# Kernel tuning notes

Hardware: AMD Instinct MI355X
Metric: run time of the kernel (lower is better)

The kernel has to match this reference:

```python
import jax, jax.numpy as jnp
import numpy as np


def _gru_layer(x, h0, W_ih, W_hh, b_ih, b_hh):
    """PyTorch-convention GRU layer.
    x: [B, T, F], h0: [B, H], W_ih: [3H, F], W_hh: [3H, H], biases: [3H].
    Gate order (torch): r, z, n.  Returns (out [B,T,H], hT [B,H]).
    """
    # Precompute input projections for all timesteps in one big GEMM.
    gx = jnp.einsum('btf,gf->btg', x, W_ih) + b_ih  # [B, T, 3H]
    gx = jnp.swapaxes(gx, 0, 1)  # [T, B, 3H] for scan

    def step(h, gx_t):
        gh = h @ W_hh.T + b_hh                      # [B, 3H]
        xr, xz, xn = jnp.split(gx_t, 3, axis=-1)
        hr, hz, hn = jnp.split(gh, 3, axis=-1)
        r = jax.nn.sigmoid(xr + hr)
        z = jax.nn.sigmoid(xz + hz)
        n = jnp.tanh(xn + r * hn)
        h_new = (1.0 - z) * n + z * h
        return h_new, h_new

    hT, outs = jax.lax.scan(step, h0, gx)
    return jnp.swapaxes(outs, 0, 1), hT  # [B, T, H], [B, H]


def setup_inputs() -> dict:
    key = jax.random.key(0)
    ks = jax.random.split(key, 12)
    B, T, F, H, O = 256, 2000, 80, 64, 29
    s = 1.0 / np.sqrt(H)  # torch GRU/Linear init scale ~ U(-1/sqrt(H), 1/sqrt(H))
    u = lambda k, shp: jax.random.uniform(k, shp, jnp.float32, -s, s)
    return {
        'x': jax.random.normal(ks[0], (B, T, F), jnp.float32),
        'h': jnp.zeros((2, B, H), jnp.float32),
        'W_ih0': u(ks[1], (3 * H, F)),
        'W_hh0': u(ks[2], (3 * H, H)),
        'b_ih0': u(ks[3], (3 * H,)),
        'b_hh0': u(ks[4], (3 * H,)),
        'W_ih1': u(ks[5], (3 * H, H)),
        'W_hh1': u(ks[6], (3 * H, H)),
        'b_ih1': u(ks[7], (3 * H,)),
        'b_hh1': u(ks[8], (3 * H,)),
        'W_fc': u(ks[9], (O, H)),
        'b_fc': u(ks[10], (O,)),
    }


def reference(x, h, W_ih0, W_hh0, b_ih0, b_hh0, W_ih1, W_hh1, b_ih1, b_hh1, W_fc, b_fc):
    # Layer 0
    out0, h0T = _gru_layer(x, h[0], W_ih0, W_hh0, b_ih0, b_hh0)
    # Layer 1 (inter-layer dropout disabled: inference / eval mode)
    out1, h1T = _gru_layer(out0, h[1], W_ih1, W_hh1, b_ih1, b_hh1)
    hidden_state = jnp.stack([h0T, h1T], axis=0)  # [num_layers, B, H]
    # fc(relu(output[:, -1]))
    logits = jax.nn.relu(out1[:, -1]) @ W_fc.T + b_fc  # [B, O]
    return logits, hidden_state
```

## Files before the change

kernel.cpp:

```cpp
#include <hip/hip_runtime.h>

#define T_STEPS 2000
#define BATCH   256
#define F_IN    80
#define HDIM    64

template<int N> struct IC { static constexpr int v = N; };

typedef _Float16 h2 __attribute__((ext_vector_type(2)));
typedef _Float16 h4 __attribute__((ext_vector_type(4)));
typedef _Float16 h8 __attribute__((ext_vector_type(8)));

union U8 { h8 v; h2 p[4]; };
union U4 { h4 v; h2 p[2]; };

__device__ __forceinline__ float sigm_f(float v) {
    float e = __expf(-v);
    return __builtin_amdgcn_rcpf(1.f + e);
}
__device__ __forceinline__ float tanh_f(float v) {
    v = fminf(fmaxf(v, -15.f), 15.f);
    float e = __expf(-2.f * v);
    return (1.f - e) * __builtin_amdgcn_rcpf(1.f + e);
}
__device__ __forceinline__ float qred(float v) {
    v += __int_as_float(__builtin_amdgcn_mov_dpp(__float_as_int(v), 0xB1, 0xF, 0xF, true));
    v += __int_as_float(__builtin_amdgcn_mov_dpp(__float_as_int(v), 0x4E, 0xF, 0xF, true));
    return v;
}
__device__ __forceinline__ void barrier_lds() {
    __builtin_amdgcn_s_waitcnt(0xC07F);
    __builtin_amdgcn_s_barrier();
}
__device__ __forceinline__ float fdot2(h2 a, h2 b, float c) {
    return __builtin_amdgcn_fdot2(a, b, c, false);
}
__device__ __forceinline__ h2 mk2(float a, float b) {
    h2 r; r.x = (_Float16)a; r.y = (_Float16)b; return r;
}

__global__ __launch_bounds__(512, 2)
void gru_fused(const float* __restrict__ x,
               const float* __restrict__ hin,
               const float* __restrict__ Wih0,
               const float* __restrict__ Whh0,
               const float* __restrict__ bih0, const float* __restrict__ bhh0,
               const float* __restrict__ Wih1,
               const float* __restrict__ Whh1,
               const float* __restrict__ bih1, const float* __restrict__ bhh1,
               float* __restrict__ out_hidden)
{
    const int b    = blockIdx.x;
    const int tid  = threadIdx.x;
    const int lane = tid & 63;
    const int w    = tid >> 6;
    const bool isL1 = (w >= 4);
    const int ks   = lane & 3;
    const int gg   = lane >> 2;
    const int jw   = ((w & 3) << 4) + gg;

    __shared__ __align__(16) _Float16 xsh[2][96];
    __shared__ __align__(16) _Float16 h0s[2][64];
    __shared__ __align__(16) _Float16 h1s[2][64];

    h2 wxr[10], wxz[10], wxn[10];
    h2 whr[8],  whz[8],  whn[8];
    float bihr, bihz, bihn, bhhr, bhhz, bhhn;
    if (!isL1) {
        const int c = ks * 20, c2 = ks * 16;
        const float* r0 = Wih0 + jw * F_IN + c;
        const float* r1 = Wih0 + (64 + jw) * F_IN + c;
        const float* r2 = Wih0 + (128 + jw) * F_IN + c;
        #pragma unroll
        for (int k = 0; k < 10; ++k) {
            wxr[k] = mk2(r0[2*k], r0[2*k+1]);
            wxz[k] = mk2(r1[2*k], r1[2*k+1]);
            wxn[k] = mk2(r2[2*k], r2[2*k+1]);
        }
        const float* s0 = Whh0 + jw * HDIM + c2;
        const float* s1 = Whh0 + (64 + jw) * HDIM + c2;
        const float* s2 = Whh0 + (128 + jw) * HDIM + c2;
        #pragma unroll
        for (int k = 0; k < 8; ++k) {
            whr[k] = mk2(s0[2*k], s0[2*k+1]);
            whz[k] = mk2(s1[2*k], s1[2*k+1]);
            whn[k] = mk2(s2[2*k], s2[2*k+1]);
        }
        bihr = bih0[jw];       bhhr = bhh0[jw];
        bihz = bih0[64 + jw];  bhhz = bhh0[64 + jw];
        bihn = bih0[128 + jw]; bhhn = bhh0[128 + jw];
    } else {
        const int c2 = ks * 16;
        const float* r0 = Wih1 + jw * HDIM + c2;
        const float* r1 = Wih1 + (64 + jw) * HDIM + c2;
        const float* r2 = Wih1 + (128 + jw) * HDIM + c2;
        const float* s0 = Whh1 + jw * HDIM + c2;
        const float* s1 = Whh1 + (64 + jw) * HDIM + c2;
        const float* s2 = Whh1 + (128 + jw) * HDIM + c2;
        #pragma unroll
        for (int k = 0; k < 8; ++k) {
            wxr[k] = mk2(r0[2*k], r0[2*k+1]);
            wxz[k] = mk2(r1[2*k], r1[2*k+1]);
            wxn[k] = mk2(r2[2*k], r2[2*k+1]);
            whr[k] = mk2(s0[2*k], s0[2*k+1]);
            whz[k] = mk2(s1[2*k], s1[2*k+1]);
            whn[k] = mk2(s2[2*k], s2[2*k+1]);
        }
        wxr[8] = mk2(0.f, 0.f); wxr[9] = mk2(0.f, 0.f);
        wxz[8] = mk2(0.f, 0.f); wxz[9] = mk2(0.f, 0.f);
        wxn[8] = mk2(0.f, 0.f); wxn[9] = mk2(0.f, 0.f);
        bihr = bih1[jw] + bhh1[jw];
        bihz = bih1[64 + jw] + bhh1[64 + jw];
        bihn = bih1[128 + jw];
        bhhn = bhh1[128 + jw];
        bhhr = 0.f; bhhz = 0.f;
    }

    float hreg = isL1 ? hin[BATCH * HDIM + b * HDIM + jw]
                      : hin[b * HDIM + jw];
    if (w == 0) {
        h0s[1][lane] = (_Float16)hin[b * HDIM + lane];
        h1s[1][lane] = (_Float16)hin[BATCH * HDIM + b * HDIM + lane];
    }
    const float* xrow = x + (size_t)b * T_STEPS * F_IN;
    const int xe = 2 * lane;
    const int xc = xe / 20, xpp = xe % 20;
    float2 xa = make_float2(0.f, 0.f), xb = make_float2(0.f, 0.f);
    if (w == 7 && lane < 40) {
        float2 v0 = ((const float2*)(xrow + 0 * F_IN))[lane];
        float2 v1 = ((const float2*)(xrow + 1 * F_IN))[lane];
        *(h2*)(&xsh[0][xc * 24 + xpp]) = mk2(v0.x, v0.y);
        *(h2*)(&xsh[1][xc * 24 + xpp]) = mk2(v1.x, v1.y);
        xa = ((const float2*)(xrow + 2 * F_IN))[lane];
        xb = ((const float2*)(xrow + 3 * F_IN))[lane];
    }
    __syncthreads();

    float gxr = 0.f, gxz = 0.f, gxn = 0.f;
    if (!isL1) {
        U8 x0, x1; U4 x2;
        x0.v = ((const h8*)(&xsh[0][ks * 24]))[0];
        x1.v = ((const h8*)(&xsh[0][ks * 24]))[1];
        x2.v = *(const h4*)(&xsh[0][ks * 24 + 16]);
        float ar = 0.f, az = 0.f, an = 0.f;
        #pragma unroll
        for (int q = 0; q < 4; ++q) {
            ar = fdot2(wxr[q], x0.p[q], ar);
            az = fdot2(wxz[q], x0.p[q], az);
            an = fdot2(wxn[q], x0.p[q], an);
        }
        #pragma unroll
        for (int q = 0; q < 4; ++q) {
            ar = fdot2(wxr[4 + q], x1.p[q], ar);
            az = fdot2(wxz[4 + q], x1.p[q], az);
            an = fdot2(wxn[4 + q], x1.p[q], an);
        }
        #pragma unroll
        for (int q = 0; q < 2; ++q) {
            ar = fdot2(wxr[8 + q], x2.p[q], ar);
            az = fdot2(wxz[8 + q], x2.p[q], az);
            an = fdot2(wxn[8 + q], x2.p[q], an);
        }
        gxr = qred(ar) + bihr; gxz = qred(az) + bihz; gxn = qred(an) + bihn;
    }

    auto step = [&](int i, auto ipc) {
        constexpr int IP = decltype(ipc)::v;
        constexpr int IO = IP ^ 1;

        if (w == 7 && lane < 40) {
            float2 v = (IP == 0) ? xa : xb;
            *(h2*)(&xsh[IP][xc * 24 + xpp]) = mk2(v.x, v.y);
            if (i <= T_STEPS - 5) {
                float2 nv = ((const float2*)(xrow + (size_t)(i + 4) * F_IN))[lane];
                if (IP == 0) xa = nv; else xb = nv;
            }
        }

        if (!isL1) {
            U8 ha, hb;
            ha.v = ((const h8*)(&h0s[IO][ks * 16]))[0];
            hb.v = ((const h8*)(&h0s[IO][ks * 16]))[1];
            U8 x0, x1; U4 x2;
            x0.v = ((const h8*)(&xsh[IO][ks * 24]))[0];
            x1.v = ((const h8*)(&xsh[IO][ks * 24]))[1];
            x2.v = *(const h4*)(&xsh[IO][ks * 24 + 16]);

            float ahr = 0.f, ahz = 0.f, ahn = 0.f;
            #pragma unroll
            for (int q = 0; q < 4; ++q) {
                ahr = fdot2(whr[q], ha.p[q], ahr);
                ahz = fdot2(whz[q], ha.p[q], ahz);
                ahn = fdot2(whn[q], ha.p[q], ahn);
            }
            #pragma unroll
            for (int q = 0; q < 4; ++q) {
                ahr = fdot2(whr[4 + q], hb.p[q], ahr);
                ahz = fdot2(whz[4 + q], hb.p[q], ahz);
                ahn = fdot2(whn[4 + q], hb.p[q], ahn);
            }
            float r = sigm_f(gxr + qred(ahr) + bhhr);
            float z = sigm_f(gxz + qred(ahz) + bhhz);
            float n = tanh_f(gxn + r * (qred(ahn) + bhhn));
            hreg = (1.f - z) * n + z * hreg;
            if (ks == 0) h0s[IP][jw] = (_Float16)hreg;

            float axr = 0.f, axz = 0.f, axn = 0.f;
            #pragma unroll
            for (int q = 0; q < 4; ++q) {
                axr = fdot2(wxr[q], x0.p[q], axr);
                axz = fdot2(wxz[q], x0.p[q], axz);
                axn = fdot2(wxn[q], x0.p[q], axn);
            }
            #pragma unroll
            for (int q = 0; q < 4; ++q) {
                axr = fdot2(wxr[4 + q], x1.p[q], axr);
                axz = fdot2(wxz[4 + q], x1.p[q], axz);
                axn = fdot2(wxn[4 + q], x1.p[q], axn);
            }
            #pragma unroll
            for (int q = 0; q < 2; ++q) {
                axr = fdot2(wxr[8 + q], x2.p[q], axr);
                axz = fdot2(wxz[8 + q], x2.p[q], axz);
                axn = fdot2(wxn[8 + q], x2.p[q], axn);
            }
            gxr = qred(axr) + bihr;
            gxz = qred(axz) + bihz;
            gxn = qred(axn) + bihn;
        } else if (i >= 1) {
            U8 aa, ab, ba, bb;
            aa.v = ((const h8*)(&h0s[IO][ks * 16]))[0];
            ab.v = ((const h8*)(&h0s[IO][ks * 16]))[1];
            ba.v = ((const h8*)(&h1s[IP][ks * 16]))[0];
            bb.v = ((const h8*)(&h1s[IP][ks * 16]))[1];
            float ar = 0.f, az = 0.f, anx = 0.f, anh = 0.f;
            #pragma unroll
            for (int q = 0; q < 4; ++q) {
                ar  = fdot2(wxr[q], aa.p[q], ar);
                az  = fdot2(wxz[q], aa.p[q], az);
                anx = fdot2(wxn[q], aa.p[q], anx);
            }
            #pragma unroll
            for (int q = 0; q < 4; ++q) {
                ar  = fdot2(wxr[4 + q], ab.p[q], ar);
                az  = fdot2(wxz[4 + q], ab.p[q], az);
                anx = fdot2(wxn[4 + q], ab.p[q], anx);
            }
            #pragma unroll
            for (int q = 0; q < 4; ++q) {
                ar  = fdot2(whr[q], ba.p[q], ar);
                az  = fdot2(whz[q], ba.p[q], az);
                anh = fdot2(whn[q], ba.p[q], anh);
            }
            #pragma unroll
            for (int q = 0; q < 4; ++q) {
                ar  = fdot2(whr[4 + q], bb.p[q], ar);
                az  = fdot2(whz[4 + q], bb.p[q], az);
                anh = fdot2(whn[4 + q], bb.p[q], anh);
            }
            float r = sigm_f(qred(ar) + bihr);
            float z = sigm_f(qred(az) + bihz);
            float n = tanh_f(qred(anx) + bihn + r * (qred(anh) + bhhn));
            hreg = (1.f - z) * n + z * hreg;
            if (ks == 0) h1s[IO][jw] = (_Float16)hreg;
        }

        barrier_lds();
    };

    for (int ii = 0; ii < T_STEPS / 2; ++ii) {
        step(2 * ii,     IC<0>{});
        step(2 * ii + 1, IC<1>{});
    }

    if (isL1) {
        U8 aa, ab, ba, bb;
        aa.v = ((const h8*)(&h0s[1][ks * 16]))[0];
        ab.v = ((const h8*)(&h0s[1][ks * 16]))[1];
        ba.v = ((const h8*)(&h1s[0][ks * 16]))[0];
        bb.v = ((const h8*)(&h1s[0][ks * 16]))[1];
        float ar = 0.f, az = 0.f, anx = 0.f, anh = 0.f;
        #pragma unroll
        for (int q = 0; q < 4; ++q) {
            ar  = fdot2(wxr[q], aa.p[q], ar);
            az  = fdot2(wxz[q], aa.p[q], az);
            anx = fdot2(wxn[q], aa.p[q], anx);
        }
        #pragma unroll
        for (int q = 0; q < 4; ++q) {
            ar  = fdot2(wxr[4 + q], ab.p[q], ar);
            az  = fdot2(wxz[4 + q], ab.p[q], az);
            anx = fdot2(wxn[4 + q], ab.p[q], anx);
        }
        #pragma unroll
        for (int q = 0; q < 4; ++q) {
            ar  = fdot2(whr[q], ba.p[q], ar);
            az  = fdot2(whz[q], ba.p[q], az);
            anh = fdot2(whn[q], ba.p[q], anh);
        }
        #pragma unroll
        for (int q = 0; q < 4; ++q) {
            ar  = fdot2(whr[4 + q], bb.p[q], ar);
            az  = fdot2(whz[4 + q], bb.p[q], az);
            anh = fdot2(whn[4 + q], bb.p[q], anh);
        }
        float r = sigm_f(qred(ar) + bihr);
        float z = sigm_f(qred(az) + bihz);
        float n = tanh_f(qred(anx) + bihn + r * (qred(anh) + bhhn));
        hreg = (1.f - z) * n + z * hreg;
    }

    if (ks == 0) {
        if (!isL1) out_hidden[b * HDIM + jw] = hreg;
        else       out_hidden[BATCH * HDIM + b * HDIM + jw] = hreg;
    }
}

__global__ void fc_kernel(const float* __restrict__ hidden,
                          const float* __restrict__ Wfc,
                          const float* __restrict__ bfc,
                          float* __restrict__ logits)
{
    const int b = blockIdx.x;
    const int o = threadIdx.x;
    if (o < 29) {
        const float* hb = hidden + BATCH * HDIM + b * HDIM;
        float acc = bfc[o];
        #pragma unroll
        for (int j = 0; j < HDIM; ++j)
            acc += fmaxf(hb[j], 0.f) * Wfc[o * HDIM + j];
        logits[b * 29 + o] = acc;
    }
}

extern "C" void kernel_launch(void* const* d_in, const int* in_sizes, int n_in,
                              void* d_out, int out_size, void* d_ws, size_t ws_size,
                              hipStream_t stream) {
    const float* x    = (const float*)d_in[0];
    const float* h    = (const float*)d_in[1];
    const float* Wih0 = (const float*)d_in[2];
    const float* Whh0 = (const float*)d_in[3];
    const float* bih0 = (const float*)d_in[4];
    const float* bhh0 = (const float*)d_in[5];
    const float* Wih1 = (const float*)d_in[6];
    const float* Whh1 = (const float*)d_in[7];
    const float* bih1 = (const float*)d_in[8];
    const float* bhh1 = (const float*)d_in[9];
    const float* Wfc  = (const float*)d_in[10];
    const float* bfc  = (const float*)d_in[11];

    float* out    = (float*)d_out;
    float* logits = out;
    float* hidden = out + BATCH * 29;

    gru_fused<<<BATCH, 512, 0, stream>>>(
        x, h, Wih0, Whh0, bih0, bhh0, Wih1, Whh1, bih1, bhh1, hidden);

    fc_kernel<<<BATCH, 64, 0, stream>>>(hidden, Wfc, bfc, logits);
}
```

Before: 1.247 ms.

## Split input projection into separate GEMM kernel and shrink scan to two waves

Moves the layer-0 input projection out of the recurrent kernel into a standalone kernel that writes fp16 gate pre-activations to workspace. The scan kernel drops to one wave per layer, where each lane owns a full hidden row and holds the whole weight row in registers, so the DPP quad reductions go away. Layer 0 keeps a 4-deep ring of hidden-state buffers so layer 1 can trail by one step. In exchange it adds an extra kernel launch and a workspace round trip of about 200MB in fp16, leaves very high register pressure (6x32 h2 in layer 1), and runs only 128 threads per block with serial dot products of length 64.

```diff
diff --git a/kernel.cpp b/kernel.cpp
--- a/kernel.cpp
+++ b/kernel.cpp
@@ -8,11 +8,9 @@
 template<int N> struct IC { static constexpr int v = N; };
 
 typedef _Float16 h2 __attribute__((ext_vector_type(2)));
-typedef _Float16 h4 __attribute__((ext_vector_type(4)));
 typedef _Float16 h8 __attribute__((ext_vector_type(8)));
 
 union U8 { h8 v; h2 p[4]; };
-union U4 { h4 v; h2 p[2]; };
 
 __device__ __forceinline__ float sigm_f(float v) {
     float e = __expf(-v);
@@ -23,11 +21,6 @@
     float e = __expf(-2.f * v);
     return (1.f - e) * __builtin_amdgcn_rcpf(1.f + e);
 }
-__device__ __forceinline__ float qred(float v) {
-    v += __int_as_float(__builtin_amdgcn_mov_dpp(__float_as_int(v), 0xB1, 0xF, 0xF, true));
-    v += __int_as_float(__builtin_amdgcn_mov_dpp(__float_as_int(v), 0x4E, 0xF, 0xF, true));
-    return v;
-}
 __device__ __forceinline__ void barrier_lds() {
     __builtin_amdgcn_s_waitcnt(0xC07F);
     __builtin_amdgcn_s_barrier();
@@ -39,280 +32,249 @@
     h2 r; r.x = (_Float16)a; r.y = (_Float16)b; return r;
 }
 
-__global__ __launch_bounds__(512, 2)
-void gru_fused(const float* __restrict__ x,
-               const float* __restrict__ hin,
-               const float* __restrict__ Wih0,
-               const float* __restrict__ Whh0,
-               const float* __restrict__ bih0, const float* __restrict__ bhh0,
-               const float* __restrict__ Wih1,
-               const float* __restrict__ Whh1,
-               const float* __restrict__ bih1, const float* __restrict__ bhh1,
-               float* __restrict__ out_hidden)
+__global__ __launch_bounds__(64, 2)
+void gx_gemm(const float* __restrict__ x,
+             const float* __restrict__ Wih0,
+             const float* __restrict__ bih0,
+             const float* __restrict__ bhh0,
+             _Float16* __restrict__ gxp)
 {
-    const int b    = blockIdx.x;
-    const int tid  = threadIdx.x;
-    const int lane = tid & 63;
-    const int w    = tid >> 6;
-    const bool isL1 = (w >= 4);
-    const int ks   = lane & 3;
-    const int gg   = lane >> 2;
-    const int jw   = ((w & 3) << 4) + gg;
-
-    __shared__ __align__(16) _Float16 xsh[2][96];
-    __shared__ __align__(16) _Float16 h0s[2][64];
-    __shared__ __align__(16) _Float16 h1s[2][64];
-
-    h2 wxr[10], wxz[10], wxn[10];
-    h2 whr[8],  whz[8],  whn[8];
-    float bihr, bihz, bihn, bhhr, bhhz, bhhn;
-    if (!isL1) {
-        const int c = ks * 20, c2 = ks * 16;
-        const float* r0 = Wih0 + jw * F_IN + c;
-        const float* r1 = Wih0 + (64 + jw) * F_IN + c;
-        const float* r2 = Wih0 + (128 + jw) * F_IN + c;
+    const int j = threadIdx.x;
+    const long total = (long)BATCH * T_STEPS;
+    const long per   = total / gridDim.x;
+    const long r0    = (long)blockIdx.x * per;
+    const long r1    = r0 + per;
+
+    h2 wr[40], wz[40], wn[40];
+    {
+        const float* a = Wih0 + (size_t)j * F_IN;
+        const float* bb = Wih0 + (size_t)(64 + j) * F_IN;
+        const float* c = Wih0 + (size_t)(128 + j) * F_IN;
         #pragma unroll
-        for (int k = 0; k < 10; ++k) {
-            wxr[k] = mk2(r0[2*k], r0[2*k+1]);
-            wxz[k] = mk2(r1[2*k], r1[2*k+1]);
-            wxn[k] = mk2(r2[2*k], r2[2*k+1]);
-        }
-        const float* s0 = Whh0 + jw * HDIM + c2;
-        const float* s1 = Whh0 + (64 + jw) * HDIM + c2;
-        const float* s2 = Whh0 + (128 + jw) * HDIM + c2;
+        for (int k = 0; k < 40; ++k) {
+            wr[k] = mk2(a[2*k],  a[2*k+1]);
+            wz[k] = mk2(bb[2*k], bb[2*k+1]);
+            wn[k] = mk2(c[2*k],  c[2*k+1]);
+        }
+    }
+    const float br = bih0[j]       + bhh0[j];
+    const float bz = bih0[64 + j]  + bhh0[64 + j];
+    const float bn = bih0[128 + j];
+
+    __shared__ __align__(16) _Float16 xs[2][80];
+
+    if (j < 40) {
+        float2 v = ((const float2*)(x + r0 * F_IN))[j];
+        *(h2*)&xs[0][2 * j] = mk2(v.x, v.y);
+    }
+    for (long r = r0; r < r1; ++r) {
+        const int cur = (int)(r - r0) & 1;
+        float2 v = make_float2(0.f, 0.f);
+        const bool pf = (j < 40) && (r + 1 < r1);
+        if (pf) v = ((const float2*)(x + (r + 1) * F_IN))[j];
+
+        U8 xv[10];
         #pragma unroll
-        for (int k = 0; k < 8; ++k) {
-            whr[k] = mk2(s0[2*k], s0[2*k+1]);
-            whz[k] = mk2(s1[2*k], s1[2*k+1]);
-            whn[k] = mk2(s2[2*k], s2[2*k+1]);
-        }
-        bihr = bih0[jw];       bhhr = bhh0[jw];
-        bihz = bih0[64 + jw];  bhhz = bhh0[64 + jw];
-        bihn = bih0[128 + jw]; bhhn = bhh0[128 + jw];
+        for (int q = 0; q < 10; ++q) xv[q].v = ((const h8*)xs[cur])[q];
+
+        float ar = br, az = bz, an = bn;
+        #pragma unroll
+        for (int q = 0; q < 10; ++q)
+            #pragma unroll
+            for (int p = 0; p < 4; ++p) {
+                ar = fdot2(wr[4*q+p], xv[q].p[p], ar);
+                az = fdot2(wz[4*q+p], xv[q].p[p], az);
+                an = fdot2(wn[4*q+p], xv[q].p[p], an);
+            }
+        _Float16* g = gxp + r * 192;
+        g[j]       = (_Float16)ar;
+        g[64 + j]  = (_Float16)az;
+        g[128 + j] = (_Float16)an;
+
+        if (pf) *(h2*)&xs[cur ^ 1][2 * j] = mk2(v.x, v.y);
+    }
+}
+
+__global__ __launch_bounds__(128, 1)
+void gru_scan(const _Float16* __restrict__ gx,
+              const float* __restrict__ hin,
+              const float* __restrict__ Whh0,
+              const float* __restrict__ bhh0,
+              const float* __restrict__ Wih1,
+              const float* __restrict__ Whh1,
+              const float* __restrict__ bih1, const float* __restrict__ bhh1,
+              float* __restrict__ out_hidden)
+{
+    const int b = blockIdx.x;
+    const int j = threadIdx.x & 63;
+    const int w = threadIdx.x >> 6;
+
+    __shared__ __align__(16) _Float16 h0r[4][64];
+    __shared__ __align__(16) _Float16 h1r[2][64];
+
+    if (w == 0) {
+        h2 whr[32], whz[32], whn[32];
+        {
+            const float* a0 = Whh0 + (size_t)j * HDIM;
+            const float* a1 = Whh0 + (size_t)(64 + j) * HDIM;
+            const float* a2 = Whh0 + (size_t)(128 + j) * HDIM;
+            #pragma unroll
+            for (int k = 0; k < 32; ++k) {
+                whr[k] = mk2(a0[2*k], a0[2*k+1]);
+                whz[k] = mk2(a1[2*k], a1[2*k+1]);
+                whn[k] = mk2(a2[2*k], a2[2*k+1]);
+            }
+        }
+        const float bn0h = bhh0[128 + j];
+        float hreg = hin[b * HDIM + j];
+        h0r[3][j] = (_Float16)hreg;
+
+        const _Float16* gbase = gx + (size_t)b * T_STEPS * 192;
+        _Float16 grf[2], gzf[2], gnf[2];
+        grf[0] = gbase[j];        gzf[0] = gbase[64 + j];        gnf[0] = gbase[128 + j];
+        grf[1] = gbase[192 + j];  gzf[1] = gbase[192 + 64 + j];  gnf[1] = gbase[192 + 128 + j];
+
+        __syncthreads();
+
+        auto stepL0 = [&](int i, auto c3) {
+            constexpr int I3 = decltype(c3)::v;
+            constexpr int IP = I3 & 1;
+            constexpr int IR = (I3 + 3) & 3;
+            U8 hv[8];
+            #pragma unroll
+            for (int q = 0; q < 8; ++q) hv[q].v = ((const h8*)h0r[IR])[q];
+            float ar  = (float)grf[IP];
+            float az  = (float)gzf[IP];
+            float gxn = (float)gnf[IP];
+            float anh = bn0h;
+            const int ipf = (i + 2 < T_STEPS) ? (i + 2) : (T_STEPS - 1);
+            const _Float16* gnx = gbase + (size_t)ipf * 192 + j;
+            grf[IP] = gnx[0]; gzf[IP] = gnx[64]; gnf[IP] = gnx[128];
+            #pragma unroll
+            for (int q = 0; q < 8; ++q)
+                #pragma unroll
+                for (int p = 0; p < 4; ++p) {
+                    ar  = fdot2(whr[4*q+p], hv[q].p[p], ar);
+                    az  = fdot2(whz[4*q+p], hv[q].p[p], az);
+                    anh = fdot2(whn[4*q+p], hv[q].p[p], anh);
+                }
+            float r = sigm_f(ar);
+            float z = sigm_f(az);
+            float n = tanh_f(gxn + r * anh);
+            hreg = (1.f - z) * n + z * hreg;
+            h0r[I3][j] = (_Float16)hreg;
+            barrier_lds();
+        };
+
+        for (int ii = 0; ii < T_STEPS / 4; ++ii) {
+            const int i = 4 * ii;
+            stepL0(i + 0, IC<0>{});
+            stepL0(i + 1, IC<1>{});
+            stepL0(i + 2, IC<2>{});
+            stepL0(i + 3, IC<3>{});
+        }
+        out_hidden[b * HDIM + j] = hreg;
     } else {
-        const int c2 = ks * 16;
-        const float* r0 = Wih1 + jw * HDIM + c2;
-        const float* r1 = Wih1 + (64 + jw) * HDIM + c2;
-        const float* r2 = Wih1 + (128 + jw) * HDIM + c2;
-        const float* s0 = Whh1 + jw * HDIM + c2;
-        const float* s1 = Whh1 + (64 + jw) * HDIM + c2;
-        const float* s2 = Whh1 + (128 + jw) * HDIM + c2;
-        #pragma unroll
-        for (int k = 0; k < 8; ++k) {
-            wxr[k] = mk2(r0[2*k], r0[2*k+1]);
-            wxz[k] = mk2(r1[2*k], r1[2*k+1]);
-            wxn[k] = mk2(r2[2*k], r2[2*k+1]);
-            whr[k] = mk2(s0[2*k], s0[2*k+1]);
-            whz[k] = mk2(s1[2*k], s1[2*k+1]);
-            whn[k] = mk2(s2[2*k], s2[2*k+1]);
-        }
-        wxr[8] = mk2(0.f, 0.f); wxr[9] = mk2(0.f, 0.f);
-        wxz[8] = mk2(0.f, 0.f); wxz[9] = mk2(0.f, 0.f);
-        wxn[8] = mk2(0.f, 0.f); wxn[9] = mk2(0.f, 0.f);
-        bihr = bih1[jw] + bhh1[jw];
-        bihz = bih1[64 + jw] + bhh1[64 + jw];
-        bihn = bih1[128 + jw];
-        bhhn = bhh1[128 + jw];
-        bhhr = 0.f; bhhz = 0.f;
-    }
-
-    float hreg = isL1 ? hin[BATCH * HDIM + b * HDIM + jw]
-                      : hin[b * HDIM + jw];
-    if (w == 0) {
-        h0s[1][lane] = (_Float16)hin[b * HDIM + lane];
-        h1s[1][lane] = (_Float16)hin[BATCH * HDIM + b * HDIM + lane];
-    }
-    const float* xrow = x + (size_t)b * T_STEPS * F_IN;
-    const int xe = 2 * lane;
-    const int xc = xe / 20, xpp = xe % 20;
-    float2 xa = make_float2(0.f, 0.f), xb = make_float2(0.f, 0.f);
-    if (w == 7 && lane < 40) {
-        float2 v0 = ((const float2*)(xrow + 0 * F_IN))[lane];
-        float2 v1 = ((const float2*)(xrow + 1 * F_IN))[lane];
-        *(h2*)(&xsh[0][xc * 24 + xpp]) = mk2(v0.x, v0.y);
-        *(h2*)(&xsh[1][xc * 24 + xpp]) = mk2(v1.x, v1.y);
-        xa = ((const float2*)(xrow + 2 * F_IN))[lane];
-        xb = ((const float2*)(xrow + 3 * F_IN))[lane];
-    }
-    __syncthreads();
-
-    float gxr = 0.f, gxz = 0.f, gxn = 0.f;
-    if (!isL1) {
-        U8 x0, x1; U4 x2;
-        x0.v = ((const h8*)(&xsh[0][ks * 24]))[0];
-        x1.v = ((const h8*)(&xsh[0][ks * 24]))[1];
-        x2.v = *(const h4*)(&xsh[0][ks * 24 + 16]);
-        float ar = 0.f, az = 0.f, an = 0.f;
-        #pragma unroll
-        for (int q = 0; q < 4; ++q) {
-            ar = fdot2(wxr[q], x0.p[q], ar);
-            az = fdot2(wxz[q], x0.p[q], az);
-            an = fdot2(wxn[q], x0.p[q], an);
-        }
-        #pragma unroll
-        for (int q = 0; q < 4; ++q) {
-            ar = fdot2(wxr[4 + q], x1.p[q], ar);
-            az = fdot2(wxz[4 + q], x1.p[q], az);
-            an = fdot2(wxn[4 + q], x1.p[q], an);
-        }
-        #pragma unroll
-        for (int q = 0; q < 2; ++q) {
-            ar = fdot2(wxr[8 + q], x2.p[q], ar);
-            az = fdot2(wxz[8 + q], x2.p[q], az);
-            an = fdot2(wxn[8 + q], x2.p[q], an);
-        }
-        gxr = qred(ar) + bihr; gxz = qred(az) + bihz; gxn = qred(an) + bihn;
-    }
-
-    auto step = [&](int i, auto ipc) {
-        constexpr int IP = decltype(ipc)::v;
-        constexpr int IO = IP ^ 1;
-
-        if (w == 7 && lane < 40) {
-            float2 v = (IP == 0) ? xa : xb;
-            *(h2*)(&xsh[IP][xc * 24 + xpp]) = mk2(v.x, v.y);
-            if (i <= T_STEPS - 5) {
-                float2 nv = ((const float2*)(xrow + (size_t)(i + 4) * F_IN))[lane];
-                if (IP == 0) xa = nv; else xb = nv;
+        h2 xr1[32], xz1[32], xn1[32], hr1[32], hz1[32], hn1[32];
+        {
+            const float* p0 = Wih1 + (size_t)j * HDIM;
+            const float* p1 = Wih1 + (size_t)(64 + j) * HDIM;
+            const float* p2 = Wih1 + (size_t)(128 + j) * HDIM;
+            const float* q0 = Whh1 + (size_t)j * HDIM;
+            const float* q1 = Whh1 + (size_t)(64 + j) * HDIM;
+            const float* q2 = Whh1 + (size_t)(128 + j) * HDIM;
+            #pragma unroll
+            for (int k = 0; k < 32; ++k) {
+                xr1[k] = mk2(p0[2*k], p0[2*k+1]);
+                xz1[k] = mk2(p1[2*k], p1[2*k+1]);
+                xn1[k] = mk2(p2[2*k], p2[2*k+1]);
+                hr1[k] = mk2(q0[2*k], q0[2*k+1]);
+                hz1[k] = mk2(q1[2*k], q1[2*k+1]);
+                hn1[k] = mk2(q2[2*k], q2[2*k+1]);
             }
         }
-
-        if (!isL1) {
-            U8 ha, hb;
-            ha.v = ((const h8*)(&h0s[IO][ks * 16]))[0];
-            hb.v = ((const h8*)(&h0s[IO][ks * 16]))[1];
-            U8 x0, x1; U4 x2;
-            x0.v = ((const h8*)(&xsh[IO][ks * 24]))[0];
-            x1.v = ((const h8*)(&xsh[IO][ks * 24]))[1];
-            x2.v = *(const h4*)(&xsh[IO][ks * 24 + 16]);
-
-            float ahr = 0.f, ahz = 0.f, ahn = 0.f;
-            #pragma unroll
-            for (int q = 0; q < 4; ++q) {
-                ahr = fdot2(whr[q], ha.p[q], ahr);
-                ahz = fdot2(whz[q], ha.p[q], ahz);
-                ahn = fdot2(whn[q], ha.p[q], ahn);
-            }
-            #pragma unroll
-            for (int q = 0; q < 4; ++q) {
-                ahr = fdot2(whr[4 + q], hb.p[q], ahr);
-                ahz = fdot2(whz[4 + q], hb.p[q], ahz);
-                ahn = fdot2(whn[4 + q], hb.p[q], ahn);
-            }
-            float r = sigm_f(gxr + qred(ahr) + bhhr);
-            float z = sigm_f(gxz + qred(ahz) + bhhz);
-            float n = tanh_f(gxn + r * (qred(ahn) + bhhn));
+        const float br1  = bih1[j] + bhh1[j];
+        const float bz1  = bih1[64 + j] + bhh1[64 + j];
+        const float bn1x = bih1[128 + j];
+        const float bn1h = bhh1[128 + j];
+        float hreg = hin[BATCH * HDIM + b * HDIM + j];
+        h1r[0][j] = (_Float16)hreg;
+
+        __syncthreads();
+
+        auto stepL1 = [&](auto c3) {
+            constexpr int I3 = decltype(c3)::v;
+            constexpr int IP = I3 & 1;
+            constexpr int IR = (I3 + 3) & 3;
+            U8 hv[8], uv[8];
+            #pragma unroll
+            for (int q = 0; q < 8; ++q) hv[q].v = ((const h8*)h0r[IR])[q];
+            #pragma unroll
+            for (int q = 0; q < 8; ++q) uv[q].v = ((const h8*)h1r[IP ^ 1])[q];
+            float ar = br1, az = bz1, anx = bn1x, anh = bn1h;
+            #pragma unroll
+            for (int q = 0; q < 8; ++q)
+                #pragma unroll
+                for (int p = 0; p < 4; ++p) {
+                    ar  = fdot2(xr1[4*q+p], hv[q].p[p], ar);
+                    az  = fdot2(xz1[4*q+p], hv[q].p[p], az);
+                    anx = fdot2(xn1[4*q+p], hv[q].p[p], anx);
+                }
+            #pragma unroll
+            for (int q = 0; q < 8; ++q)
+                #pragma unroll
+                for (int p = 0; p < 4; ++p) {
+                    ar  = fdot2(hr1[4*q+p], uv[q].p[p], ar);
+                    az  = fdot2(hz1[4*q+p], uv[q].p[p], az);
+                    anh = fdot2(hn1[4*q+p], uv[q].p[p], anh);
+                }
+            float r = sigm_f(ar);
+            float z = sigm_f(az);
+            float n = tanh_f(anx + r * anh);
             hreg = (1.f - z) * n + z * hreg;
-            if (ks == 0) h0s[IP][jw] = (_Float16)hreg;
-
-            float axr = 0.f, axz = 0.f, axn = 0.f;
-            #pragma unroll
-            for (int q = 0; q < 4; ++q) {
-                axr = fdot2(wxr[q], x0.p[q], axr);
-                axz = fdot2(wxz[q], x0.p[q], axz);
-                axn = fdot2(wxn[q], x0.p[q], axn);
-            }
-            #pragma unroll
-            for (int q = 0; q < 4; ++q) {
-                axr = fdot2(wxr[4 + q], x1.p[q], axr);
-                axz = fdot2(wxz[4 + q], x1.p[q], axz);
-                axn = fdot2(wxn[4 + q], x1.p[q], axn);
-            }
-            #pragma unroll
-            for (int q = 0; q < 2; ++q) {
-                axr = fdot2(wxr[8 + q], x2.p[q], axr);
-                axz = fdot2(wxz[8 + q], x2.p[q], axz);
-                axn = fdot2(wxn[8 + q], x2.p[q], axn);
-            }
-            gxr = qred(axr) + bihr;
-            gxz = qred(axz) + bihz;
-            gxn = qred(axn) + bihn;
-        } else if (i >= 1) {
-            U8 aa, ab, ba, bb;
-            aa.v = ((const h8*)(&h0s[IO][ks * 16]))[0];
-            ab.v = ((const h8*)(&h0s[IO][ks * 16]))[1];
-            ba.v = ((const h8*)(&h1s[IP][ks * 16]))[0];
-            bb.v = ((const h8*)(&h1s[IP][ks * 16]))[1];
-            float ar = 0.f, az = 0.f, anx = 0.f, anh = 0.f;
-            #pragma unroll
-            for (int q = 0; q < 4; ++q) {
-                ar  = fdot2(wxr[q], aa.p[q], ar);
-                az  = fdot2(wxz[q], aa.p[q], az);
-                anx = fdot2(wxn[q], aa.p[q], anx);
-            }
-            #pragma unroll
-            for (int q = 0; q < 4; ++q) {
-                ar  = fdot2(wxr[4 + q], ab.p[q], ar);
-                az  = fdot2(wxz[4 + q], ab.p[q], az);
-                anx = fdot2(wxn[4 + q], ab.p[q], anx);
-            }
-            #pragma unroll
-            for (int q = 0; q < 4; ++q) {
-                ar  = fdot2(whr[q], ba.p[q], ar);
-                az  = fdot2(whz[q], ba.p[q], az);
-                anh = fdot2(whn[q], ba.p[q], anh);
-            }
-            #pragma unroll
-            for (int q = 0; q < 4; ++q) {
-                ar  = fdot2(whr[4 + q], bb.p[q], ar);
-                az  = fdot2(whz[4 + q], bb.p[q], az);
-                anh = fdot2(whn[4 + q], bb.p[q], anh);
-            }
-            float r = sigm_f(qred(ar) + bihr);
-            float z = sigm_f(qred(az) + bihz);
-            float n = tanh_f(qred(anx) + bihn + r * (qred(anh) + bhhn));
+            h1r[IP][j] = (_Float16)hreg;
+            barrier_lds();
+        };
+
+        barrier_lds();
+        stepL1(IC<1>{});
+        stepL1(IC<2>{});
+        stepL1(IC<3>{});
+        for (int ii = 1; ii < T_STEPS / 4; ++ii) {
+            stepL1(IC<0>{});
+            stepL1(IC<1>{});
+            stepL1(IC<2>{});
+            stepL1(IC<3>{});
+        }
+        {
+            U8 hv[8], uv[8];
+            #pragma unroll
+            for (int q = 0; q < 8; ++q) hv[q].v = ((const h8*)h0r[3])[q];
+            #pragma unroll
+            for (int q = 0; q < 8; ++q) uv[q].v = ((const h8*)h1r[1])[q];
+            float ar = br1, az = bz1, anx = bn1x, anh = bn1h;
+            #pragma unroll
+            for (int q = 0; q < 8; ++q)
+                #pragma unroll
+                for (int p = 0; p < 4; ++p) {
+                    ar  = fdot2(xr1[4*q+p], hv[q].p[p], ar);
+                    az  = fdot2(xz1[4*q+p], hv[q].p[p], az);
+                    anx = fdot2(xn1[4*q+p], hv[q].p[p], anx);
+                }
+            #pragma unroll
+            for (int q = 0; q < 8; ++q)
+                #pragma unroll
+                for (int p = 0; p < 4; ++p) {
+                    ar  = fdot2(hr1[4*q+p], uv[q].p[p], ar);
+                    az  = fdot2(hz1[4*q+p], uv[q].p[p], az);
+                    anh = fdot2(hn1[4*q+p], uv[q].p[p], anh);
+                }
+            float r = sigm_f(ar);
+            float z = sigm_f(az);
+            float n = tanh_f(anx + r * anh);
             hreg = (1.f - z) * n + z * hreg;
-            if (ks == 0) h1s[IO][jw] = (_Float16)hreg;
-        }
-
-        barrier_lds();
-    };
-
-    for (int ii = 0; ii < T_STEPS / 2; ++ii) {
-        step(2 * ii,     IC<0>{});
-        step(2 * ii + 1, IC<1>{});
-    }
-
-    if (isL1) {
-        U8 aa, ab, ba, bb;
-        aa.v = ((const h8*)(&h0s[1][ks * 16]))[0];
-        ab.v = ((const h8*)(&h0s[1][ks * 16]))[1];
-        ba.v = ((const h8*)(&h1s[0][ks * 16]))[0];
-        bb.v = ((const h8*)(&h1s[0][ks * 16]))[1];
-        float ar = 0.f, az = 0.f, anx = 0.f, anh = 0.f;
-        #pragma unroll
-        for (int q = 0; q < 4; ++q) {
-            ar  = fdot2(wxr[q], aa.p[q], ar);
-            az  = fdot2(wxz[q], aa.p[q], az);
-            anx = fdot2(wxn[q], aa.p[q], anx);
-        }
-        #pragma unroll
-        for (int q = 0; q < 4; ++q) {
-            ar  = fdot2(wxr[4 + q], ab.p[q], ar);
-            az  = fdot2(wxz[4 + q], ab.p[q], az);
-            anx = fdot2(wxn[4 + q], ab.p[q], anx);
-        }
-        #pragma unroll
-        for (int q = 0; q < 4; ++q) {
-            ar  = fdot2(whr[q], ba.p[q], ar);
-            az  = fdot2(whz[q], ba.p[q], az);
-            anh = fdot2(whn[q], ba.p[q], anh);
-        }
-        #pragma unroll
-        for (int q = 0; q < 4; ++q) {
-            ar  = fdot2(whr[4 + q], bb.p[q], ar);
-            az  = fdot2(whz[4 + q], bb.p[q], az);
-            anh = fdot2(whn[4 + q], bb.p[q], anh);
-        }
-        float r = sigm_f(qred(ar) + bihr);
-        float z = sigm_f(qred(az) + bihz);
-        float n = tanh_f(qred(anx) + bihn + r * (qred(anh) + bhhn));
-        hreg = (1.f - z) * n + z * hreg;
-    }
-
-    if (ks == 0) {
-        if (!isL1) out_hidden[b * HDIM + jw] = hreg;
-        else       out_hidden[BATCH * HDIM + b * HDIM + jw] = hreg;
+        }
+        out_hidden[BATCH * HDIM + b * HDIM + j] = hreg;
     }
 }
 
@@ -353,8 +315,10 @@
     float* logits = out;
     float* hidden = out + BATCH * 29;
 
-    gru_fused<<<BATCH, 512, 0, stream>>>(
-        x, h, Wih0, Whh0, bih0, bhh0, Wih1, Whh1, bih1, bhh1, hidden);
-
+    _Float16* gxp = (_Float16*)d_ws;
+
+    gx_gemm<<<2048, 64, 0, stream>>>(x, Wih0, bih0, bhh0, gxp);
+    gru_scan<<<BATCH, 128, 0, stream>>>(
+        gxp, h, Whh0, bhh0, Wih1, Whh1, bih1, bhh1, hidden);
     fc_kernel<<<BATCH, 64, 0, stream>>>(hidden, Wfc, bfc, logits);
 }
```

Result: slower. 1.482 ms (+18.9%).
